# Optimization experiments

Hardware: AMD Instinct MI355X
Metric: run time of the kernel (lower is better)

Reference implementation:

```python
import jax, jax.numpy as jnp
import numpy as np
import math

D_MODEL = 768
N_HEADS = 12
B, S = 2, 2048


def setup_inputs() -> dict:
    key = jax.random.key(0)
    ks = jax.random.split(key, 12)
    q = jax.random.normal(ks[0], (B, S, D_MODEL), dtype=jnp.float32)
    k = jax.random.normal(ks[1], (B, S, D_MODEL), dtype=jnp.float32)
    v = jax.random.normal(ks[2], (B, S, D_MODEL), dtype=jnp.float32)
    # 2D causal mask (0 = masked), exercising the mask.dim()==2 branch
    mask = jnp.tril(jnp.ones((S, S), dtype=jnp.int32))
    sc = 1.0 / math.sqrt(D_MODEL)
    wq = jax.random.normal(ks[3], (D_MODEL, D_MODEL), dtype=jnp.float32) * sc
    wk = jax.random.normal(ks[4], (D_MODEL, D_MODEL), dtype=jnp.float32) * sc
    wv = jax.random.normal(ks[5], (D_MODEL, D_MODEL), dtype=jnp.float32) * sc
    wo = jax.random.normal(ks[6], (D_MODEL, D_MODEL), dtype=jnp.float32) * sc
    bq = jnp.zeros((D_MODEL,), jnp.float32)
    bk = jnp.zeros((D_MODEL,), jnp.float32)
    bv = jnp.zeros((D_MODEL,), jnp.float32)
    bo = jnp.zeros((D_MODEL,), jnp.float32)
    return {"query": q, "key": k, "value": v, "mask": mask,
            "wq": wq, "bq": bq, "wk": wk, "bk": bk,
            "wv": wv, "bv": bv, "wo": wo, "bo": bo}


def reference(query, key, value, mask, wq, bq, wk, bk, wv, bv, wo, bo):
    b, sq, d = query.shape
    h = N_HEADS
    dk = d // h
    scale = math.sqrt(dk)

    def proj(x, w, bias):  # torch Linear: x @ W^T + b, then split heads -> [b,h,s,dk]
        y = x @ w.T + bias
        return y.reshape(b, -1, h, dk).transpose(0, 2, 1, 3)

    Q = proj(query, wq, bq)
    K = proj(key, wk, bk)
    V = proj(value, wv, bv)

    scores = jnp.einsum('bhqd,bhkd->bhqk', Q, K) / scale  # [b,h,sq,sk]
    scores = jnp.where(mask[None, None, :, :] == 0, jnp.float32(-1e9), scores)
    attn = jax.nn.softmax(scores, axis=-1)  # dropout p=0 (eval): identity
    ctx = jnp.einsum('bhqk,bhkd->bhqd', attn, V)
    ctx = ctx.transpose(0, 2, 1, 3).reshape(b, sq, d)
    out = ctx @ wo.T + bo
    return out, attn
```

## Files before the change

kernel.cpp:

```cpp
#include <hip/hip_runtime.h>

#define D_MODEL 768
#define N_HEADS 12
#define DK      64
#define BB      2
#define SS      2048
#define PH      (BB*SS*D_MODEL)
#define WN      (D_MODEL*D_MODEL)

typedef short bf8_t   __attribute__((ext_vector_type(8)));
typedef float f32x4   __attribute__((ext_vector_type(4)));

__device__ __forceinline__ unsigned short f2b(float f) {
  unsigned u = __builtin_bit_cast(unsigned, f);
  unsigned r = (u + 0x7FFFu + ((u >> 16) & 1u)) >> 16;
  return (unsigned short)r;
}
__device__ __forceinline__ unsigned pk2(float a, float b) {
  return (unsigned)f2b(a) | ((unsigned)f2b(b) << 16);
}
__device__ __forceinline__ f32x4 mfma16(bf8_t a, bf8_t b, f32x4 c) {
  return __builtin_amdgcn_mfma_f32_16x16x32_bf16(a, b, c, 0, 0, 0);
}

__device__ __forceinline__ bf8_t ld_frag64(const unsigned short* t, int rbase, int kk, int lane) {
  int row = rbase + (lane & 15);
  int k = (kk << 5) + ((lane >> 4) << 3);
  uint4 u = *(const uint4*)&t[(row << 6) + (k ^ ((row & 7) << 3))];
  return __builtin_bit_cast(bf8_t, u);
}

__device__ __forceinline__ void st_tile_pair(unsigned short* lds, int r0, int k8, uint4 a0, uint4 a1) {
  int sw = ((k8 ^ (r0 & 7)) << 3);
  *(uint4*)&lds[(r0 << 6) + sw] = a0;
  *(uint4*)&lds[((r0 + 32) << 6) + sw] = a1;
}

__device__ __forceinline__ void mma_step(const unsigned short* As, const unsigned short* Ws,
                                         int w, int lane, f32x4 acc[4]) {
#pragma unroll
  for (int kk = 0; kk < 2; ++kk) {
    bf8_t a = ld_frag64(As, w << 4, kk, lane);
#pragma unroll
    for (int n = 0; n < 4; ++n)
      acc[n] = mfma16(a, ld_frag64(Ws, n << 4, kk, lane), acc[n]);
  }
}

__global__ __launch_bounds__(256)
void prep(const float* __restrict__ q, const float* __restrict__ k, const float* __restrict__ v,
          const float* __restrict__ wq, const float* __restrict__ wk,
          const float* __restrict__ wv, const float* __restrict__ wo,
          unsigned short* __restrict__ dst) {
  const int QKV_C = PH / 8;
  const int W_C   = WN / 8;
  const int TOTAL = 3 * QKV_C + 4 * W_C;
  for (int c = blockIdx.x * 256 + threadIdx.x; c < TOTAL; c += gridDim.x * 256) {
    const float* s;
    int off;
    if (c < 3 * QKV_C) {
      int seg = c / QKV_C; off = c - seg * QKV_C;
      s = seg == 0 ? q : seg == 1 ? k : v;
    } else {
      int c2 = c - 3 * QKV_C;
      int seg = c2 / W_C; off = c2 - seg * W_C;
      s = seg == 0 ? wq : seg == 1 ? wk : seg == 2 ? wv : wo;
    }
    const float* p = s + (size_t)off * 8;
    float4 a = *(const float4*)p;
    float4 b = *(const float4*)(p + 4);
    uint4 o;
    o.x = pk2(a.x, a.y); o.y = pk2(a.z, a.w);
    o.z = pk2(b.x, b.y); o.w = pk2(b.z, b.w);
    *(uint4*)&dst[(size_t)c * 8] = o;
  }
}

__global__ __launch_bounds__(256)
void qkv_proj(const unsigned short* __restrict__ Qc, const unsigned short* __restrict__ Kc,
              const unsigned short* __restrict__ Vc,
              const unsigned short* __restrict__ Wq, const unsigned short* __restrict__ Wk,
              const unsigned short* __restrict__ Wv,
              const float* __restrict__ bq, const float* __restrict__ bk,
              const float* __restrict__ bv,
              unsigned short* __restrict__ Qh, unsigned short* __restrict__ Kh,
              unsigned short* __restrict__ VT) {
  __shared__ __align__(16) unsigned short As[4096];
  __shared__ __align__(16) unsigned short Ws[4096];
  const int tid = threadIdx.x, lane = tid & 63, w = tid >> 6;
  const int g = lane >> 4, qc = lane & 15;
  const int p = blockIdx.x;
  const int l = (p & 7) * 288 + (p >> 3);
  const int z = l / 768, rr = l % 768;
  const int m0 = (rr / 12) << 6, n0 = (rr % 12) << 6;

  const unsigned short* A = z == 0 ? Qc : z == 1 ? Kc : Vc;
  const unsigned short* W = z == 0 ? Wq : z == 1 ? Wk : Wv;
  const float* bias = z == 0 ? bq : z == 1 ? bk : bv;
  const float oscale = z == 0 ? 0.125f : 1.0f;

  const int r0 = tid >> 3, k8 = tid & 7;
  const unsigned short* Ab0 = A + (size_t)(m0 + r0) * D_MODEL + (k8 << 3);
  const unsigned short* Ab1 = Ab0 + 32 * D_MODEL;
  const unsigned short* Wb0 = W + (size_t)(n0 + r0) * D_MODEL + (k8 << 3);
  const unsigned short* Wb1 = Wb0 + 32 * D_MODEL;

  uint4 ra0 = *(const uint4*)Ab0, ra1 = *(const uint4*)Ab1;
  uint4 rw0 = *(const uint4*)Wb0, rw1 = *(const uint4*)Wb1;

  f32x4 acc[4] = {};
  for (int kt = 0; kt < 12; ++kt) {
    __syncthreads();
    st_tile_pair(As, r0, k8, ra0, ra1);
    st_tile_pair(Ws, r0, k8, rw0, rw1);
    __syncthreads();
    if (kt < 11) {
      int off = (kt + 1) << 6;
      ra0 = *(const uint4*)(Ab0 + off); ra1 = *(const uint4*)(Ab1 + off);
      rw0 = *(const uint4*)(Wb0 + off); rw1 = *(const uint4*)(Wb1 + off);
    }
    mma_step(As, Ws, w, lane, acc);
  }

  const int wrow = (w << 4) + (g << 2);
  const int b = m0 >> 11;
  const int h = n0 >> 6;
  if (z < 2) {
    unsigned short* dst = (z == 0 ? Qh : Kh) + ((size_t)(b * N_HEADS + h)) * SS * DK;
#pragma unroll
    for (int n = 0; n < 4; ++n) {
      int col = (n << 4) + qc;
      float bb = bias[n0 + col];
#pragma unroll
      for (int r = 0; r < 4; ++r) {
        int s = (m0 + wrow + r) & (SS - 1);
        dst[(size_t)s * DK + col] = f2b((acc[n][r] + bb) * oscale);
      }
    }
  } else {
    unsigned short* dst = VT + ((size_t)(b * N_HEADS + h)) * DK * SS;
#pragma unroll
    for (int n = 0; n < 4; ++n) {
      int col = (n << 4) + qc;
      float bb = bias[n0 + col];
      int s = (m0 + wrow) & (SS - 1);
      ushort4 pk;
      pk.x = f2b(acc[n][0] + bb); pk.y = f2b(acc[n][1] + bb);
      pk.z = f2b(acc[n][2] + bb); pk.w = f2b(acc[n][3] + bb);
      *(ushort4*)&dst[(size_t)col * SS + s] = pk;
    }
  }
}

__global__ __launch_bounds__(256)
void attn4(const unsigned short* __restrict__ Qh, const unsigned short* __restrict__ Kh,
           const unsigned short* __restrict__ VT,
           float* __restrict__ attn, unsigned short* __restrict__ ctx) {
  __shared__ __align__(16) unsigned short Ks[4096];
  __shared__ __align__(16) unsigned short Vts[4096];
  __shared__ __align__(16) unsigned short Pw[4][1024];

  const int tid = threadIdx.x, lane = tid & 63, w = tid >> 6;
  const int g = lane >> 4, qc = lane & 15;
  const int p = blockIdx.x;
  const int l = (p & 7) * 96 + (p >> 3);
  const int bh = l >> 5;
  const int x = l & 31;
  const int qt = (x & 1) ? (31 - (x >> 1)) : (x >> 1);
  const int q0 = qt << 6;
  const int b = bh / N_HEADS, h = bh - b * N_HEADS;

  const unsigned short* Qb = Qh + (size_t)bh * SS * DK;
  const unsigned short* Kb = Kh + (size_t)bh * SS * DK;
  const unsigned short* Vb = VT + (size_t)bh * DK * SS;
  float* attn_b = attn + (size_t)bh * SS * SS;

  bf8_t qf0, qf1;
  {
    const unsigned short* qp = &Qb[(size_t)(q0 + (w << 4) + qc) * DK + (g << 3)];
    qf0 = __builtin_bit_cast(bf8_t, *(const uint4*)qp);
    qf1 = __builtin_bit_cast(bf8_t, *(const uint4*)(qp + 32));
  }

  const int r0 = tid >> 3, k8 = tid & 7;
  auto ldK = [&](int t, uint4& a0, uint4& a1) {
    const unsigned short* bse = Kb + ((size_t)t << 12);
    a0 = *(const uint4*)&bse[(r0 << 6) + (k8 << 3)];
    a1 = *(const uint4*)&bse[((r0 + 32) << 6) + (k8 << 3)];
  };
  auto ldV = [&](int t, uint4& a0, uint4& a1) {
    const unsigned short* bse = Vb + (t << 6);
    a0 = *(const uint4*)&bse[(size_t)r0 * SS + (k8 << 3)];
    a1 = *(const uint4*)&bse[(size_t)(r0 + 32) * SS + (k8 << 3)];
  };

  const int qglob = q0 + (w << 4) + qc;
  float psum = 0.f;

  {
    uint4 ka0, ka1;
    ldK(0, ka0, ka1);
    for (int t = 0; t <= qt; ++t) {
      __syncthreads();
      st_tile_pair(Ks, r0, k8, ka0, ka1);
      __syncthreads();
      if (t < qt) ldK(t + 1, ka0, ka1);
      f32x4 sc[4] = {};
#pragma unroll
      for (int kk = 0; kk < 2; ++kk) {
        bf8_t qf = kk ? qf1 : qf0;
#pragma unroll
        for (int n = 0; n < 4; ++n)
          sc[n] = mfma16(ld_frag64(Ks, n << 4, kk, lane), qf, sc[n]);
      }
      const bool diag = (t == qt);
      const int kbase = (t << 6) + (g << 2);
#pragma unroll
      for (int n = 0; n < 4; ++n) {
#pragma unroll
        for (int r = 0; r < 4; ++r) {
          int k = kbase + (n << 4) + r;
          bool ok = !diag || (k <= qglob);
          psum += ok ? __expf(sc[n][r]) : 0.f;
        }
      }
    }
  }
  psum += __shfl_xor(psum, 16);
  psum += __shfl_xor(psum, 32);
  const float Linv = 1.0f / psum;

  f32x4 ct[4] = {};
  unsigned short* myP = Pw[w];
  {
    uint4 ka0, ka1, va0, va1;
    ldK(0, ka0, ka1);
    ldV(0, va0, va1);
    for (int t = 0; t <= qt; ++t) {
      __syncthreads();
      st_tile_pair(Ks, r0, k8, ka0, ka1);
      st_tile_pair(Vts, r0, k8, va0, va1);
      __syncthreads();
      if (t < qt) { ldK(t + 1, ka0, ka1); ldV(t + 1, va0, va1); }
      f32x4 sc[4] = {};
#pragma unroll
      for (int kk = 0; kk < 2; ++kk) {
        bf8_t qf = kk ? qf1 : qf0;
#pragma unroll
        for (int n = 0; n < 4; ++n)
          sc[n] = mfma16(ld_frag64(Ks, n << 4, kk, lane), qf, sc[n]);
      }
      const bool diag = (t == qt);
      const int k0 = t << 6;
#pragma unroll
      for (int n = 0; n < 4; ++n) {
        int klocal = (n << 4) + (g << 2);
        int kb = k0 + klocal;
        float pr[4];
#pragma unroll
        for (int r = 0; r < 4; ++r) {
          bool ok = !diag || (kb + r <= qglob);
          pr[r] = ok ? __expf(sc[n][r]) * Linv : 0.f;
        }
        float4 pv;
        pv.x = pr[0]; pv.y = pr[1]; pv.z = pr[2]; pv.w = pr[3];
        *(float4*)&attn_b[(size_t)qglob * SS + kb] = pv;
        uint2 pk;
        pk.x = pk2(pr[0], pr[1]);
        pk.y = pk2(pr[2], pr[3]);
        *(uint2*)&myP[(qc << 6) + (klocal ^ ((qc & 7) << 3))] = pk;
      }
      asm volatile("s_waitcnt lgkmcnt(0)" ::: "memory");
      __builtin_amdgcn_sched_barrier(0);
#pragma unroll
      for (int kk = 0; kk < 2; ++kk) {
        bf8_t pf = ld_frag64(myP, 0, kk, lane);
#pragma unroll
        for (int n = 0; n < 4; ++n)
          ct[n] = mfma16(pf, ld_frag64(Vts, n << 4, kk, lane), ct[n]);
      }
    }
  }

  {
    const int zr = tid >> 4;
    const int zc = (tid & 15) << 2;
    const float4 z4 = {0.f, 0.f, 0.f, 0.f};
    for (int c0 = q0 + 64; c0 < SS; c0 += 64) {
#pragma unroll
      for (int i = 0; i < 4; ++i)
        *(float4*)&attn_b[(size_t)(q0 + zr + (i << 4)) * SS + c0 + zc] = z4;
    }
  }

  const int wrow = (w << 4) + (g << 2);
#pragma unroll
  for (int n = 0; n < 4; ++n) {
#pragma unroll
    for (int r = 0; r < 4; ++r) {
      int m = q0 + wrow + r;
      int col = (n << 4) + qc;
      ctx[((size_t)(b * SS + m)) * D_MODEL + h * DK + col] = f2b(ct[n][r]);
    }
  }
}

__global__ __launch_bounds__(256)
void out_proj(const unsigned short* __restrict__ A, const unsigned short* __restrict__ W,
              const float* __restrict__ bias, float* __restrict__ out) {
  __shared__ __align__(16) unsigned short As[4096];
  __shared__ __align__(16) unsigned short Ws[4096];
  const int tid = threadIdx.x, lane = tid & 63, w = tid >> 6;
  const int g = lane >> 4, qc = lane & 15;
  const int p = blockIdx.x;
  const int l = (p & 7) * 96 + (p >> 3);
  const int m0 = (l / 12) << 6, n0 = (l % 12) << 6;

  const int r0 = tid >> 3, k8 = tid & 7;
  const unsigned short* Ab0 = A + (size_t)(m0 + r0) * D_MODEL + (k8 << 3);
  const unsigned short* Ab1 = Ab0 + 32 * D_MODEL;
  const unsigned short* Wb0 = W + (size_t)(n0 + r0) * D_MODEL + (k8 << 3);
  const unsigned short* Wb1 = Wb0 + 32 * D_MODEL;

  uint4 ra0 = *(const uint4*)Ab0, ra1 = *(const uint4*)Ab1;
  uint4 rw0 = *(const uint4*)Wb0, rw1 = *(const uint4*)Wb1;

  f32x4 acc[4] = {};
  for (int kt = 0; kt < 12; ++kt) {
    __syncthreads();
    st_tile_pair(As, r0, k8, ra0, ra1);
    st_tile_pair(Ws, r0, k8, rw0, rw1);
    __syncthreads();
    if (kt < 11) {
      int off = (kt + 1) << 6;
      ra0 = *(const uint4*)(Ab0 + off); ra1 = *(const uint4*)(Ab1 + off);
      rw0 = *(const uint4*)(Wb0 + off); rw1 = *(const uint4*)(Wb1 + off);
    }
    mma_step(As, Ws, w, lane, acc);
  }

  const int wrow = (w << 4) + (g << 2);
#pragma unroll
  for (int n = 0; n < 4; ++n) {
    int col = n0 + (n << 4) + qc;
    float bb = bias[col];
#pragma unroll
    for (int r = 0; r < 4; ++r)
      out[(size_t)(m0 + wrow + r) * D_MODEL + col] = acc[n][r] + bb;
  }
}

extern "C" void kernel_launch(void* const* d_in, const int* in_sizes, int n_in,
                              void* d_out, int out_size, void* d_ws, size_t ws_size,
                              hipStream_t stream) {
  const float* q  = (const float*)d_in[0];
  const float* k  = (const float*)d_in[1];
  const float* v  = (const float*)d_in[2];
  const float* wq = (const float*)d_in[4];
  const float* bq = (const float*)d_in[5];
  const float* wk = (const float*)d_in[6];
  const float* bk = (const float*)d_in[7];
  const float* wv = (const float*)d_in[8];
  const float* bv = (const float*)d_in[9];
  const float* wo = (const float*)d_in[10];
  const float* bo = (const float*)d_in[11];

  float* out  = (float*)d_out;
  float* attn = out + (size_t)BB * SS * D_MODEL;

  unsigned short* wsu = (unsigned short*)d_ws;
  unsigned short* Qc  = wsu;
  unsigned short* Kc  = Qc + PH;
  unsigned short* Vc  = Kc + PH;
  unsigned short* Wqb = Vc + PH;
  unsigned short* Wkb = Wqb + WN;
  unsigned short* Wvb = Wkb + WN;
  unsigned short* Wob = Wvb + WN;
  unsigned short* Qhd = Wob + WN;
  unsigned short* Khd = Qhd + PH;
  unsigned short* VTw = Khd + PH;
  unsigned short* Cw  = VTw + PH;

  dim3 blk(256);
  prep<<<2048, blk, 0, stream>>>(q, k, v, wq, wk, wv, wo, wsu);
  qkv_proj<<<2304, blk, 0, stream>>>(Qc, Kc, Vc, Wqb, Wkb, Wvb, bq, bk, bv, Qhd, Khd, VTw);
  attn4<<<768, blk, 0, stream>>>(Qhd, Khd, VTw, attn, Cw);
  out_proj<<<768, blk, 0, stream>>>(Cw, Wob, bo, out);
}
```

Measured before the change: 172.0 us.

## Enlarge QKV projection tiles to 128x128 with 2x2 warp grid

The QKV projection kernel now uses 128x128 output tiles with each of four waves computing a 64x64 sub-tile (16 MFMA accumulators), replacing 64x64 tiles with one 16-row strip per wave. The concatenated Wq/Wk/Wv buffer is indexed as one 2304-row matrix, so a tile selects its input by column segment. This raises arithmetic intensity per LDS and global load and cuts the grid from 2304 to 576 blocks. In exchange it uses more registers and LDS per block, and fewer blocks may leave some CUs idle or reduce latency hiding.

```diff
diff --git a/kernel.cpp b/kernel.cpp
--- a/kernel.cpp
+++ b/kernel.cpp
@@ -28,6 +28,10 @@
   int k = (kk << 5) + ((lane >> 4) << 3);
   uint4 u = *(const uint4*)&t[(row << 6) + (k ^ ((row & 7) << 3))];
   return __builtin_bit_cast(bf8_t, u);
+}
+
+__device__ __forceinline__ void st_row(unsigned short* lds, int rr, int k8, uint4 a) {
+  *(uint4*)&lds[(rr << 6) + ((k8 ^ (rr & 7)) << 3)] = a;
 }
 
 __device__ __forceinline__ void st_tile_pair(unsigned short* lds, int r0, int k8, uint4 a0, uint4 a1) {
@@ -77,77 +81,106 @@
 }
 
 __global__ __launch_bounds__(256)
-void qkv_proj(const unsigned short* __restrict__ Qc, const unsigned short* __restrict__ Kc,
-              const unsigned short* __restrict__ Vc,
-              const unsigned short* __restrict__ Wq, const unsigned short* __restrict__ Wk,
-              const unsigned short* __restrict__ Wv,
-              const float* __restrict__ bq, const float* __restrict__ bk,
-              const float* __restrict__ bv,
-              unsigned short* __restrict__ Qh, unsigned short* __restrict__ Kh,
-              unsigned short* __restrict__ VT) {
-  __shared__ __align__(16) unsigned short As[4096];
-  __shared__ __align__(16) unsigned short Ws[4096];
+void qkv_proj2(const unsigned short* __restrict__ Qc, const unsigned short* __restrict__ Kc,
+               const unsigned short* __restrict__ Vc,
+               const unsigned short* __restrict__ Wcat,
+               const float* __restrict__ bq, const float* __restrict__ bk,
+               const float* __restrict__ bv,
+               unsigned short* __restrict__ Qh, unsigned short* __restrict__ Kh,
+               unsigned short* __restrict__ VT) {
+  __shared__ __align__(16) unsigned short As[128 * 64];
+  __shared__ __align__(16) unsigned short Bs[128 * 64];
   const int tid = threadIdx.x, lane = tid & 63, w = tid >> 6;
   const int g = lane >> 4, qc = lane & 15;
+  const int wm = w >> 1, wn = w & 1;
   const int p = blockIdx.x;
-  const int l = (p & 7) * 288 + (p >> 3);
-  const int z = l / 768, rr = l % 768;
-  const int m0 = (rr / 12) << 6, n0 = (rr % 12) << 6;
+  const int l = (p & 7) * 72 + (p >> 3);
+  const int m0 = (l / 18) << 7;
+  const int n0 = (l % 18) << 7;
+  const int z = n0 / D_MODEL;
+  const int nseg = n0 - z * D_MODEL;
 
   const unsigned short* A = z == 0 ? Qc : z == 1 ? Kc : Vc;
-  const unsigned short* W = z == 0 ? Wq : z == 1 ? Wk : Wv;
   const float* bias = z == 0 ? bq : z == 1 ? bk : bv;
-  const float oscale = z == 0 ? 0.125f : 1.0f;
 
   const int r0 = tid >> 3, k8 = tid & 7;
-  const unsigned short* Ab0 = A + (size_t)(m0 + r0) * D_MODEL + (k8 << 3);
-  const unsigned short* Ab1 = Ab0 + 32 * D_MODEL;
-  const unsigned short* Wb0 = W + (size_t)(n0 + r0) * D_MODEL + (k8 << 3);
-  const unsigned short* Wb1 = Wb0 + 32 * D_MODEL;
-
-  uint4 ra0 = *(const uint4*)Ab0, ra1 = *(const uint4*)Ab1;
-  uint4 rw0 = *(const uint4*)Wb0, rw1 = *(const uint4*)Wb1;
-
-  f32x4 acc[4] = {};
+  const unsigned short* Ab = A + (size_t)(m0 + r0) * D_MODEL + (k8 << 3);
+  const unsigned short* Bb = Wcat + (size_t)(n0 + r0) * D_MODEL + (k8 << 3);
+
+  uint4 ra[4], rb[4];
+#pragma unroll
+  for (int i = 0; i < 4; ++i) {
+    ra[i] = *(const uint4*)(Ab + (size_t)(i * 32) * D_MODEL);
+    rb[i] = *(const uint4*)(Bb + (size_t)(i * 32) * D_MODEL);
+  }
+
+  f32x4 acc[4][4] = {};
   for (int kt = 0; kt < 12; ++kt) {
     __syncthreads();
-    st_tile_pair(As, r0, k8, ra0, ra1);
-    st_tile_pair(Ws, r0, k8, rw0, rw1);
+#pragma unroll
+    for (int i = 0; i < 4; ++i) {
+      st_row(As, r0 + i * 32, k8, ra[i]);
+      st_row(Bs, r0 + i * 32, k8, rb[i]);
+    }
     __syncthreads();
     if (kt < 11) {
       int off = (kt + 1) << 6;
-      ra0 = *(const uint4*)(Ab0 + off); ra1 = *(const uint4*)(Ab1 + off);
-      rw0 = *(const uint4*)(Wb0 + off); rw1 = *(const uint4*)(Wb1 + off);
-    }
-    mma_step(As, Ws, w, lane, acc);
-  }
-
-  const int wrow = (w << 4) + (g << 2);
-  const int b = m0 >> 11;
-  const int h = n0 >> 6;
+#pragma unroll
+      for (int i = 0; i < 4; ++i) {
+        ra[i] = *(const uint4*)(Ab + (size_t)(i * 32) * D_MODEL + off);
+        rb[i] = *(const uint4*)(Bb + (size_t)(i * 32) * D_MODEL + off);
+      }
+    }
+#pragma unroll
+    for (int kk = 0; kk < 2; ++kk) {
+      bf8_t am[4], bn[4];
+#pragma unroll
+      for (int i = 0; i < 4; ++i) am[i] = ld_frag64(As, (wm << 6) + (i << 4), kk, lane);
+#pragma unroll
+      for (int j = 0; j < 4; ++j) bn[j] = ld_frag64(Bs, (wn << 6) + (j << 4), kk, lane);
+#pragma unroll
+      for (int i = 0; i < 4; ++i)
+#pragma unroll
+        for (int j = 0; j < 4; ++j)
+          acc[i][j] = mfma16(am[i], bn[j], acc[i][j]);
+    }
+  }
+
+  const int rbase = m0 + (wm << 6) + (g << 2);
   if (z < 2) {
-    unsigned short* dst = (z == 0 ? Qh : Kh) + ((size_t)(b * N_HEADS + h)) * SS * DK;
-#pragma unroll
-    for (int n = 0; n < 4; ++n) {
-      int col = (n << 4) + qc;
-      float bb = bias[n0 + col];
-#pragma unroll
-      for (int r = 0; r < 4; ++r) {
-        int s = (m0 + wrow + r) & (SS - 1);
-        dst[(size_t)s * DK + col] = f2b((acc[n][r] + bb) * oscale);
+    unsigned short* dstb = (z == 0 ? Qh : Kh);
+    const float oscale = z == 0 ? 0.125f : 1.0f;
+#pragma unroll
+    for (int j = 0; j < 4; ++j) {
+      int cseg = nseg + (wn << 6) + (j << 4) + qc;
+      int h = cseg >> 6, d = cseg & 63;
+      float bb = bias[cseg];
+#pragma unroll
+      for (int i = 0; i < 4; ++i) {
+#pragma unroll
+        for (int r = 0; r < 4; ++r) {
+          int row = rbase + (i << 4) + r;
+          int b = row >> 11, s = row & (SS - 1);
+          dstb[(((size_t)(b * N_HEADS + h)) * SS + s) * DK + d] =
+              f2b((acc[i][j][r] + bb) * oscale);
+        }
       }
     }
   } else {
-    unsigned short* dst = VT + ((size_t)(b * N_HEADS + h)) * DK * SS;
-#pragma unroll
-    for (int n = 0; n < 4; ++n) {
-      int col = (n << 4) + qc;
-      float bb = bias[n0 + col];
-      int s = (m0 + wrow) & (SS - 1);
-      ushort4 pk;
-      pk.x = f2b(acc[n][0] + bb); pk.y = f2b(acc[n][1] + bb);
-      pk.z = f2b(acc[n][2] + bb); pk.w = f2b(acc[n][3] + bb);
-      *(ushort4*)&dst[(size_t)col * SS + s] = pk;
+#pragma unroll
+    for (int j = 0; j < 4; ++j) {
+      int cseg = nseg + (wn << 6) + (j << 4) + qc;
+      int h = cseg >> 6, d = cseg & 63;
+      float bb = bias[cseg];
+#pragma unroll
+      for (int i = 0; i < 4; ++i) {
+        int row = rbase + (i << 4);
+        int b = row >> 11, s = row & (SS - 1);
+        ushort4 pk;
+        pk.x = f2b(acc[i][j][0] + bb); pk.y = f2b(acc[i][j][1] + bb);
+        pk.z = f2b(acc[i][j][2] + bb); pk.w = f2b(acc[i][j][3] + bb);
+        *(ushort4*)&VT[(((size_t)(b * N_HEADS + h)) * DK + d) * SS + s] = pk;
+      }
     }
   }
 }
@@ -383,7 +416,7 @@
 
   dim3 blk(256);
   prep<<<2048, blk, 0, stream>>>(q, k, v, wq, wk, wv, wo, wsu);
-  qkv_proj<<<2304, blk, 0, stream>>>(Qc, Kc, Vc, Wqb, Wkb, Wvb, bq, bk, bv, Qhd, Khd, VTw);
+  qkv_proj2<<<576, blk, 0, stream>>>(Qc, Kc, Vc, Wqb, bq, bk, bv, Qhd, Khd, VTw);
   attn4<<<768, blk, 0, stream>>>(Qhd, Khd, VTw, attn, Cw);
   out_proj<<<768, blk, 0, stream>>>(Cw, Wob, bo, out);
 }
```

New measurement: 178.0 us. 1.04x slower.
